# Kernel optimization log

Measured on AMD Instinct MI355X. Metric: run time of the kernel, lower is better.

## Reference

```python
import jax, jax.numpy as jnp
import numpy as np

B, S, D_MODEL = 2, 2048, 1024
HEADS = 16
DK = D_MODEL // HEADS  # 64
Q_RANK, RANK = 6, 2
ROPE_BASE = 10000.0


def _xavier(key, shape):
    # torch nn.init.xavier_uniform_ on weight (out,in); stored here as (in,out)
    fan_in, fan_out = shape
    a = (6.0 / (fan_in + fan_out)) ** 0.5
    return jax.random.uniform(key, shape, jnp.float32, -a, a)


def setup_inputs() -> dict:
    key = jax.random.key(0)
    ks = jax.random.split(key, 10)
    inp = {
        "q": jax.random.normal(ks[0], (B, S, D_MODEL), jnp.float32),
        "k": jax.random.normal(ks[1], (B, S, D_MODEL), jnp.float32),
        "v": jax.random.normal(ks[2], (B, S, D_MODEL), jnp.float32),
        # causal mask; mask==0 -> -inf in scores
        "mask": jnp.tril(jnp.ones((S, S), dtype=bool))[None, None],
        "W_Aq": _xavier(ks[3], (D_MODEL, Q_RANK * HEADS)),
        "W_Ak": _xavier(ks[4], (D_MODEL, RANK * HEADS)),
        "W_Av": _xavier(ks[5], (D_MODEL, RANK * HEADS)),
        "W_Bq": _xavier(ks[6], (D_MODEL, Q_RANK * DK)),
        "W_Bk": _xavier(ks[7], (D_MODEL, RANK * DK)),
        "W_Bv": _xavier(ks[8], (D_MODEL, RANK * DK)),
        "Wo": _xavier(ks[9], (D_MODEL, D_MODEL)),
    }
    return inp


def _rotary_cos_sin(seq_len, dim):
    inv_freq = 1.0 / (ROPE_BASE ** (jnp.arange(0, dim, 2, dtype=jnp.float32) / dim))
    freqs = jnp.outer(jnp.arange(seq_len, dtype=jnp.float32), inv_freq)  # [S, dim/2]
    return jnp.cos(freqs)[None, :, None, :], jnp.sin(freqs)[None, :, None, :]


def _apply_rotary(x, cos, sin):
    # x: [B, S, R, dk]; rotate-half style RoPE
    d = x.shape[-1] // 2
    x1, x2 = x[..., :d], x[..., d:]
    return jnp.concatenate([x1 * cos + x2 * sin, -x1 * sin + x2 * cos], axis=-1)


def reference(q, k, v, mask, W_Aq, W_Ak, W_Av, W_Bq, W_Bk, W_Bv, Wo):
    Bn, Sn, D = q.shape
    # low-rank factor projections
    A_q = (q @ W_Aq).reshape(Bn, Sn, HEADS, Q_RANK)
    A_k = (k @ W_Ak).reshape(Bn, Sn, HEADS, RANK)
    A_v = (v @ W_Av).reshape(Bn, Sn, HEADS, RANK)
    B_q = (q @ W_Bq).reshape(Bn, Sn, Q_RANK, DK)
    B_k = (k @ W_Bk).reshape(Bn, Sn, RANK, DK)
    B_v = (v @ W_Bv).reshape(Bn, Sn, RANK, DK)
    cos, sin = _rotary_cos_sin(Sn, DK)
    B_q = _apply_rotary(B_q, cos, sin)
    B_k = _apply_rotary(B_k, cos, sin)
    # reconstruct per-head q/k/v: [B,H,S,dk]
    qh = jnp.einsum("bshr,bsrd->bhsd", A_q, B_q) / Q_RANK
    kh = jnp.einsum("bshr,bsrd->bhsd", A_k, B_k) / RANK
    vh = jnp.einsum("bshr,bsrd->bhsd", A_v, B_v) / RANK
    # NOTE: original divides by d_k (not sqrt(d_k)) -- faithful to source
    score = jnp.einsum("bhqd,bhkd->bhqk", qh, kh) / DK
    score = jnp.where(mask, score, -jnp.inf)
    # dropout is identity (eval / dropout=0.0)
    att = jax.nn.softmax(score, axis=-1)
    out = jnp.einsum("bhqk,bhkd->bqhd", att, vh).reshape(Bn, Sn, D)
    return out @ Wo
```

## Files before the change

kernel.cpp:

```cpp
#include <hip/hip_runtime.h>
#include <hip/hip_bf16.h>


typedef __attribute__((ext_vector_type(8))) short short8;
typedef __attribute__((ext_vector_type(4))) float floatx4;

#define MFMA16(a, b, c) __builtin_amdgcn_mfma_f32_16x16x32_bf16(a, b, c, 0, 0, 0)

__device__ __forceinline__ float b2f(short s) {
    unsigned int u = ((unsigned int)(unsigned short)s) << 16;
    float f; __builtin_memcpy(&f, &u, 4); return f;
}
__device__ __forceinline__ unsigned short bfbits(float x) {
    __hip_bfloat16 h = __float2bfloat16(x);
    unsigned short u; __builtin_memcpy(&u, &h, 2); return u;
}

__device__ __forceinline__ float wsrc(int n, int k,
                                      const float* __restrict__ Aq, const float* __restrict__ Bq,
                                      const float* __restrict__ Ak, const float* __restrict__ Bk,
                                      const float* __restrict__ Av, const float* __restrict__ Bv,
                                      const float* __restrict__ Wo) {
    if (n < 96) return Aq[(size_t)k * 96 + n];
    if (n < 480) return Bq[(size_t)k * 384 + (n - 96)];
    if (n < 512) return 0.f;
    if (n < 544) return Ak[(size_t)k * 32 + (n - 512)];
    if (n < 672) return Bk[(size_t)k * 128 + (n - 544)];
    if (n < 768) return 0.f;
    if (n < 800) return Av[(size_t)k * 32 + (n - 768)];
    if (n < 928) return Bv[(size_t)k * 128 + (n - 800)];
    if (n < 1024) return 0.f;
    return Wo[(size_t)k * 1024 + (n - 1024)];
}

__global__ __launch_bounds__(256) void pack_wT_kernel(const float* __restrict__ Aq,
                                                      const float* __restrict__ Bq,
                                                      const float* __restrict__ Ak,
                                                      const float* __restrict__ Bk,
                                                      const float* __restrict__ Av,
                                                      const float* __restrict__ Bv,
                                                      const float* __restrict__ Wo,
                                                      __hip_bfloat16* __restrict__ outBase) {
    __shared__ float tile[64][65];
    int k0 = blockIdx.x * 64, n0 = blockIdx.y * 64;
    int tid = threadIdx.x;
#pragma unroll
    for (int p = 0; p < 16; ++p) {
        int idx = p * 256 + tid;
        int kl = idx >> 6, nl = idx & 63;
        tile[kl][nl] = wsrc(n0 + nl, k0 + kl, Aq, Bq, Ak, Bk, Av, Bv, Wo);
    }
    __syncthreads();
#pragma unroll
    for (int p = 0; p < 4; ++p) {
        int idx = p * 256 + tid;
        int nl = idx >> 4, kq = (idx & 15) * 4;
        ushort4 o;
        o.x = bfbits(tile[kq][nl]);
        o.y = bfbits(tile[kq + 1][nl]);
        o.z = bfbits(tile[kq + 2][nl]);
        o.w = bfbits(tile[kq + 3][nl]);
        *(ushort4*)&outBase[(size_t)(n0 + nl) * 1024 + k0 + kq] = o;
    }
}

__global__ __launch_bounds__(256) void gemm3_kernel(const float* __restrict__ q,
                                                    const float* __restrict__ k,
                                                    const float* __restrict__ v,
                                                    const __hip_bfloat16* __restrict__ WT,
                                                    __hip_bfloat16* __restrict__ Pq,
                                                    __hip_bfloat16* __restrict__ Pk,
                                                    __hip_bfloat16* __restrict__ Pv) {
    __shared__ __align__(16) __hip_bfloat16 As[64][72];
    __shared__ __align__(16) __hip_bfloat16 Bs[128][72];
    int lin = blockIdx.x;
    int t = (lin >> 3) & 7;
    int mi = (lin & 7) + ((lin >> 6) << 3);
    int m0 = mi * 64;
    const float* A; __hip_bfloat16* C; int N, n0, wrow;
    if (t < 4)      { A = q; C = Pq; N = 512; n0 = t * 128;        wrow = t * 128; }
    else if (t < 6) { A = k; C = Pk; N = 256; n0 = (t - 4) * 128;  wrow = 512 + (t - 4) * 128; }
    else            { A = v; C = Pv; N = 256; n0 = (t - 6) * 128;  wrow = 768 + (t - 6) * 128; }
    int tid = threadIdx.x;
    int wave = tid >> 6, lane = tid & 63, quad = lane >> 4, l15 = lane & 15;
    floatx4 acc[4][2];
#pragma unroll
    for (int mt = 0; mt < 4; ++mt)
#pragma unroll
        for (int nt = 0; nt < 2; ++nt) acc[mt][nt] = (floatx4){0.f, 0.f, 0.f, 0.f};

    for (int k0 = 0; k0 < 1024; k0 += 64) {
#pragma unroll
        for (int pp = 0; pp < 4; ++pp) {
            int idx = pp * 256 + tid;
            int row = idx >> 4, c4 = (idx & 15) * 4;
            float4 av = *(const float4*)(A + (size_t)(m0 + row) * 1024 + k0 + c4);
            ushort4 bv;
            bv.x = bfbits(av.x); bv.y = bfbits(av.y); bv.z = bfbits(av.z); bv.w = bfbits(av.w);
            *(ushort4*)&As[row][c4] = bv;
        }
#pragma unroll
        for (int pp = 0; pp < 4; ++pp) {
            int idx = pp * 256 + tid;
            int row = idx >> 3, c8 = (idx & 7) * 8;
            *(uint4*)&Bs[row][c8] = *(const uint4*)(WT + (size_t)(wrow + row) * 1024 + k0 + c8);
        }
        __syncthreads();
#pragma unroll
        for (int ks = 0; ks < 64; ks += 32) {
            short8 af[4], bf[2];
#pragma unroll
            for (int mt = 0; mt < 4; ++mt)
                af[mt] = *(const short8*)&As[mt * 16 + l15][ks + quad * 8];
#pragma unroll
            for (int nt = 0; nt < 2; ++nt)
                bf[nt] = *(const short8*)&Bs[wave * 32 + nt * 16 + l15][ks + quad * 8];
#pragma unroll
            for (int mt = 0; mt < 4; ++mt)
#pragma unroll
                for (int nt = 0; nt < 2; ++nt)
                    acc[mt][nt] = MFMA16(af[mt], bf[nt], acc[mt][nt]);
        }
        __syncthreads();
    }
#pragma unroll
    for (int mt = 0; mt < 4; ++mt)
#pragma unroll
        for (int nt = 0; nt < 2; ++nt)
#pragma unroll
            for (int r = 0; r < 4; ++r) {
                int row = m0 + mt * 16 + quad * 4 + r;
                int col = n0 + wave * 32 + nt * 16 + l15;
                C[(size_t)row * N + col] = __float2bfloat16(acc[mt][nt][r]);
            }
}

__global__ __launch_bounds__(256) void gemm_out_kernel(const __hip_bfloat16* __restrict__ A,
                                                       const __hip_bfloat16* __restrict__ BT,
                                                       float* __restrict__ C) {
    __shared__ __align__(16) __hip_bfloat16 As[64][72];
    __shared__ __align__(16) __hip_bfloat16 Bs[128][72];
    int lin = blockIdx.x;
    int n0 = ((lin >> 3) & 7) * 128;
    int mi = (lin & 7) + ((lin >> 6) << 3);
    int m0 = mi * 64;
    int tid = threadIdx.x;
    int wave = tid >> 6, lane = tid & 63, quad = lane >> 4, l15 = lane & 15;
    floatx4 acc[4][2];
#pragma unroll
    for (int mt = 0; mt < 4; ++mt)
#pragma unroll
        for (int nt = 0; nt < 2; ++nt) acc[mt][nt] = (floatx4){0.f, 0.f, 0.f, 0.f};

    for (int k0 = 0; k0 < 1024; k0 += 64) {
#pragma unroll
        for (int pp = 0; pp < 2; ++pp) {
            int idx = pp * 256 + tid;
            int row = idx >> 3, c8 = (idx & 7) * 8;
            *(uint4*)&As[row][c8] = *(const uint4*)(A + (size_t)(m0 + row) * 1024 + k0 + c8);
        }
#pragma unroll
        for (int pp = 0; pp < 4; ++pp) {
            int idx = pp * 256 + tid;
            int row = idx >> 3, c8 = (idx & 7) * 8;
            *(uint4*)&Bs[row][c8] = *(const uint4*)(BT + (size_t)(n0 + row) * 1024 + k0 + c8);
        }
        __syncthreads();
#pragma unroll
        for (int ks = 0; ks < 64; ks += 32) {
            short8 af[4], bf[2];
#pragma unroll
            for (int mt = 0; mt < 4; ++mt)
                af[mt] = *(const short8*)&As[mt * 16 + l15][ks + quad * 8];
#pragma unroll
            for (int nt = 0; nt < 2; ++nt)
                bf[nt] = *(const short8*)&Bs[wave * 32 + nt * 16 + l15][ks + quad * 8];
#pragma unroll
            for (int mt = 0; mt < 4; ++mt)
#pragma unroll
                for (int nt = 0; nt < 2; ++nt)
                    acc[mt][nt] = MFMA16(af[mt], bf[nt], acc[mt][nt]);
        }
        __syncthreads();
    }
#pragma unroll
    for (int mt = 0; mt < 4; ++mt)
#pragma unroll
        for (int nt = 0; nt < 2; ++nt)
#pragma unroll
            for (int r = 0; r < 4; ++r) {
                int row = m0 + mt * 16 + quad * 4 + r;
                int col = n0 + wave * 32 + nt * 16 + l15;
                C[(size_t)row * 1024 + col] = acc[mt][nt][r];
            }
}

__global__ __launch_bounds__(256) void combine_vt_kernel(const __hip_bfloat16* __restrict__ Pq,
                                                         const __hip_bfloat16* __restrict__ Pk,
                                                         const __hip_bfloat16* __restrict__ Pv,
                                                         __hip_bfloat16* __restrict__ qh,
                                                         __hip_bfloat16* __restrict__ kh,
                                                         __hip_bfloat16* __restrict__ vT) {
    __shared__ __align__(16) __hip_bfloat16 LAq[16][96];
    __shared__ __align__(16) __hip_bfloat16 LAk[16][32];
    __shared__ __align__(16) __hip_bfloat16 LAv[16][32];
    __shared__ __align__(16) __hip_bfloat16 LBq[16][6][72];
    __shared__ __align__(16) __hip_bfloat16 LBk[16][2][72];
    __shared__ __align__(16) __hip_bfloat16 LBv[16][2][72];
    int tid = threadIdx.x;
    int token0 = blockIdx.x * 16;
    int b = token0 >> 11, s0 = token0 & 2047, bh0 = b * 16;

    for (int i = tid; i < 16 * 512; i += 256) {
        int s = i >> 9, c = i & 511;
        __hip_bfloat16 val = Pq[(size_t)(token0 + s) * 512 + c];
        if (c < 96) LAq[s][c] = val;
        else if (c < 480) LBq[s][(c - 96) >> 6][(c - 96) & 63] = val;
    }
    for (int i = tid; i < 16 * 256; i += 256) {
        int s = i >> 8, c = i & 255;
        __hip_bfloat16 vk = Pk[(size_t)(token0 + s) * 256 + c];
        __hip_bfloat16 vv = Pv[(size_t)(token0 + s) * 256 + c];
        if (c < 32) { LAk[s][c] = vk; LAv[s][c] = vv; }
        else if (c < 160) {
            LBk[s][(c - 32) >> 6][(c - 32) & 63] = vk;
            LBv[s][(c - 32) >> 6][(c - 32) & 63] = vv;
        }
    }
    __syncthreads();
    for (int i = tid; i < 4096; i += 256) {
        int s = i >> 8, rr = (i >> 5) & 7, d = i & 31;
        float inv = __expf(-(float)d * 0.28782313662425576f);
        float rev = (float)(s0 + s) * inv * 0.15915494309189535f;
        rev -= floorf(rev);
        float sn = __builtin_amdgcn_sinf(rev);
        float cs = __builtin_amdgcn_cosf(rev);
        if (rr < 6) {
            float x1 = b2f(*(short*)&LBq[s][rr][d]), x2 = b2f(*(short*)&LBq[s][rr][d + 32]);
            LBq[s][rr][d] = __float2bfloat16(x1 * cs + x2 * sn);
            LBq[s][rr][d + 32] = __float2bfloat16(-x1 * sn + x2 * cs);
        } else {
            int r2 = rr - 6;
            float x1 = b2f(*(short*)&LBk[s][r2][d]), x2 = b2f(*(short*)&LBk[s][r2][d + 32]);
            LBk[s][r2][d] = __float2bfloat16(x1 * cs + x2 * sn);
            LBk[s][r2][d + 32] = __float2bfloat16(-x1 * sn + x2 * cs);
        }
    }
    __syncthreads();
    const float QSCALE = 1.4426950408889634f / 768.0f;
    {
        int s = tid >> 4, h = tid & 15;
        float aq[6], ak0, ak1;
#pragma unroll
        for (int r = 0; r < 6; ++r) aq[r] = b2f(*(short*)&LAq[s][h * 6 + r]);
        ak0 = b2f(*(short*)&LAk[s][h * 2]);
        ak1 = b2f(*(short*)&LAk[s][h * 2 + 1]);
        size_t obase = ((size_t)(bh0 + h) * 2048 + s0 + s) * 64;
#pragma unroll
        for (int dc = 0; dc < 64; dc += 8) {
            float accq[8] = {0, 0, 0, 0, 0, 0, 0, 0};
#pragma unroll
            for (int r = 0; r < 6; ++r) {
                short8 bq = *(const short8*)&LBq[s][r][dc];
#pragma unroll
                for (int e = 0; e < 8; ++e) accq[e] += aq[r] * b2f(bq[e]);
            }
            short8 bk0 = *(const short8*)&LBk[s][0][dc];
            short8 bk1 = *(const short8*)&LBk[s][1][dc];
            ushort outq[8], outk[8];
#pragma unroll
            for (int e = 0; e < 8; ++e) {
                outq[e] = bfbits(accq[e] * QSCALE);
                outk[e] = bfbits(ak0 * b2f(bk0[e]) + ak1 * b2f(bk1[e]));
            }
            *(uint4*)((__hip_bfloat16*)qh + obase + dc) = *(uint4*)outq;
            *(uint4*)((__hip_bfloat16*)kh + obase + dc) = *(uint4*)outk;
        }
    }
    {
        int s = tid & 15, dg = tid >> 4;
#pragma unroll
        for (int h = 0; h < 16; ++h) {
            float a0 = b2f(*(short*)&LAv[s][h * 2]) * 0.5f;
            float a1 = b2f(*(short*)&LAv[s][h * 2 + 1]) * 0.5f;
#pragma unroll
            for (int dd = 0; dd < 4; ++dd) {
                int d = dg * 4 + dd;
                float val = a0 * b2f(*(short*)&LBv[s][0][d]) + a1 * b2f(*(short*)&LBv[s][1][d]);
                vT[((size_t)(bh0 + h) * 64 + d) * 2048 + s0 + s] = __float2bfloat16(val);
            }
        }
    }
}

__global__ __launch_bounds__(512) void flash_kernel(const __hip_bfloat16* __restrict__ qh,
                                                    const __hip_bfloat16* __restrict__ kh,
                                                    const __hip_bfloat16* __restrict__ vT,
                                                    __hip_bfloat16* __restrict__ att) {
    int lin = blockIdx.x + (blockIdx.y << 5);
    int bh = ((lin & 7) << 2) | ((lin >> 3) & 3);
    int tpair = lin >> 5;
    int tid = threadIdx.x;
    int wave = tid >> 6, lane = tid & 63, quad = lane >> 4, l15 = lane & 15;
    int grp = wave >> 2, wv = wave & 3;
    __shared__ __align__(16) __hip_bfloat16 Ks[2][64][72];
    __shared__ __align__(16) __hip_bfloat16 Vts[2][64][72];
    float* cb = (float*)&Ks[0][0][0];

    int row = tid >> 3, col = (tid & 7) * 8;
    const size_t khb = (size_t)bh * 2048 * 64;
    const size_t vtb = (size_t)bh * 64 * 2048;
    uint4 sk0, sk1, sv0, sv1;
#define FL_ISSUE(P)                                                                  \
    {                                                                                \
        int k0_ = (P) * 128;                                                         \
        sk0 = *(const uint4*)(kh + khb + (size_t)(k0_ + row) * 64 + col);            \
        sk1 = *(const uint4*)(kh + khb + (size_t)(k0_ + 64 + row) * 64 + col);       \
        sv0 = *(const uint4*)(vT + vtb + (size_t)row * 2048 + k0_ + col);            \
        sv1 = *(const uint4*)(vT + vtb + (size_t)row * 2048 + k0_ + 64 + col);       \
    }

    for (int pass = 0; pass < 2; ++pass) {
        int qi = pass ? tpair : (31 - tpair);
        int q0 = qi * 64;
        int npairs = (qi + 2) >> 1;
        const __hip_bfloat16* qrow =
            qh + ((size_t)bh * 2048 + q0 + wv * 16 + l15) * 64 + quad * 8;
        short8 aq0 = *(const short8*)(qrow);
        short8 aq1 = *(const short8*)(qrow + 32);

        floatx4 o[4];
#pragma unroll
        for (int nt = 0; nt < 4; ++nt) o[nt] = (floatx4){0.f, 0.f, 0.f, 0.f};
        float rs = 0.f;
        int qloc = wv * 16 + l15;

        FL_ISSUE(0);
        for (int p = 0; p < npairs; ++p) {
            __syncthreads();
            *(uint4*)&Ks[0][row][col] = sk0;
            *(uint4*)&Ks[1][row][col] = sk1;
            *(uint4*)&Vts[0][row][col] = sv0;
            *(uint4*)&Vts[1][row][col] = sv1;
            __syncthreads();
            if (p + 1 < npairs) FL_ISSUE(p + 1);

            int mytile = 2 * p + grp;
            if (mytile <= qi) {
                floatx4 s[4];
#pragma unroll
                for (int nt = 0; nt < 4; ++nt) s[nt] = (floatx4){0.f, 0.f, 0.f, 0.f};
                __builtin_amdgcn_s_setprio(1);
#pragma unroll
                for (int nt = 0; nt < 4; ++nt) {
                    short8 bk0 = *(const short8*)&Ks[grp][nt * 16 + l15][quad * 8];
                    short8 bk1 = *(const short8*)&Ks[grp][nt * 16 + l15][32 + quad * 8];
                    s[nt] = MFMA16(bk0, aq0, s[nt]);
                    s[nt] = MFMA16(bk1, aq1, s[nt]);
                }
                __builtin_amdgcn_s_setprio(0);
                if (mytile == qi) {
#pragma unroll
                    for (int nt = 0; nt < 4; ++nt) {
                        int kbase = nt * 16 + quad * 4;
#pragma unroll
                        for (int r = 0; r < 4; ++r)
                            if (kbase + r > qloc) s[nt][r] = -__builtin_inff();
                    }
                }
                float pv[4][4];
#pragma unroll
                for (int nt = 0; nt < 4; ++nt)
#pragma unroll
                    for (int r = 0; r < 4; ++r) {
                        pv[nt][r] = exp2f(s[nt][r]);
                        rs += pv[nt][r];
                    }
                union { ushort u[8]; short8 v; } p0, p1;
#pragma unroll
                for (int r = 0; r < 4; ++r) {
                    p0.u[r]     = bfbits(pv[0][r]);
                    p0.u[4 + r] = bfbits(pv[1][r]);
                    p1.u[r]     = bfbits(pv[2][r]);
                    p1.u[4 + r] = bfbits(pv[3][r]);
                }
                __builtin_amdgcn_s_setprio(1);
#pragma unroll
                for (int nt = 0; nt < 4; ++nt) {
                    int vr = nt * 16 + l15;
                    union { ushort4 h[2]; short8 v; } x0, x1;
                    x0.h[0] = *(const ushort4*)&Vts[grp][vr][quad * 4];
                    x0.h[1] = *(const ushort4*)&Vts[grp][vr][16 + quad * 4];
                    x1.h[0] = *(const ushort4*)&Vts[grp][vr][32 + quad * 4];
                    x1.h[1] = *(const ushort4*)&Vts[grp][vr][48 + quad * 4];
                    o[nt] = MFMA16(x0.v, p0.v, o[nt]);
                    o[nt] = MFMA16(x1.v, p1.v, o[nt]);
                }
                __builtin_amdgcn_s_setprio(0);
            }
        }
        __syncthreads();
        int cbase = (wv * 64 + lane) * 17;
        if (grp == 1) {
#pragma unroll
            for (int nt = 0; nt < 4; ++nt)
#pragma unroll
                for (int r = 0; r < 4; ++r) cb[cbase + nt * 4 + r] = o[nt][r];
            cb[cbase + 16] = rs;
        }
        __syncthreads();
        if (grp == 0) {
#pragma unroll
            for (int nt = 0; nt < 4; ++nt)
#pragma unroll
                for (int r = 0; r < 4; ++r) o[nt][r] += cb[cbase + nt * 4 + r];
            rs += cb[cbase + 16];
            rs += __shfl_xor(rs, 16, 64);
            rs += __shfl_xor(rs, 32, 64);
            float inv = 1.0f / rs;
            int b = bh >> 4, h = bh & 15;
            size_t obase = ((size_t)b * 2048 + q0 + wv * 16 + l15) * 1024 + h * 64 + quad * 4;
#pragma unroll
            for (int nt = 0; nt < 4; ++nt) {
                ushort ow[4];
#pragma unroll
                for (int r = 0; r < 4; ++r) ow[r] = bfbits(o[nt][r] * inv);
                *(ushort4*)((__hip_bfloat16*)att + obase + nt * 16) = *(ushort4*)ow;
            }
        }
    }
#undef FL_ISSUE
}

extern "C" void kernel_launch(void* const* d_in, const int* in_sizes, int n_in,
                              void* d_out, int out_size, void* d_ws, size_t ws_size,
                              hipStream_t stream) {
    const float* q = (const float*)d_in[0];
    const float* k = (const float*)d_in[1];
    const float* v = (const float*)d_in[2];
    const float* W_Aq = (const float*)d_in[4];
    const float* W_Ak = (const float*)d_in[5];
    const float* W_Av = (const float*)d_in[6];
    const float* W_Bq = (const float*)d_in[7];
    const float* W_Bk = (const float*)d_in[8];
    const float* W_Bv = (const float*)d_in[9];
    const float* Wo = (const float*)d_in[10];
    float* out = (float*)d_out;

    char* w = (char*)d_ws;
    __hip_bfloat16* qh  = (__hip_bfloat16*)(w + 0);
    __hip_bfloat16* kh  = (__hip_bfloat16*)(w + 8388608);
    __hip_bfloat16* vT  = (__hip_bfloat16*)(w + 16777216);
    __hip_bfloat16* WT  = (__hip_bfloat16*)(w + 25165824);
    __hip_bfloat16* WoT = WT + (size_t)1024 * 1024;
    __hip_bfloat16* Pq  = (__hip_bfloat16*)(w + 29360128);
    __hip_bfloat16* Pk  = (__hip_bfloat16*)(w + 33554432);
    __hip_bfloat16* Pv  = (__hip_bfloat16*)(w + 35651584);
    __hip_bfloat16* att = (__hip_bfloat16*)(w + 37748736);

    pack_wT_kernel<<<dim3(16, 32), 256, 0, stream>>>(W_Aq, W_Bq, W_Ak, W_Bk, W_Av, W_Bv, Wo, WT);
    gemm3_kernel<<<512, 256, 0, stream>>>(q, k, v, WT, Pq, Pk, Pv);
    combine_vt_kernel<<<256, 256, 0, stream>>>(Pq, Pk, Pv, qh, kh, vT);
    flash_kernel<<<dim3(32, 16), 512, 0, stream>>>(qh, kh, vT, att);
    gemm_out_kernel<<<512, 256, 0, stream>>>(att, WoT, out);
}
```

Baseline: 227.1 us.

## Halve GEMM M-tiles and combine token blocks to double grid sizes, vectorize combine loads

The projection and output GEMMs now use 32-row M tiles instead of 64, doubling the block count to 1024 so the 256 CUs are better filled; block-index swizzling is changed to match. The combine kernel handles 8 tokens per block instead of 16, doubling its grid, and its scalar shared-memory staging loads become 16-byte vector loads. The cost is less reuse of each B tile per block, which raises total weight traffic through L2 and LDS, and lower MFMA work per synchronization.

```diff
diff --git a/kernel.cpp b/kernel.cpp
--- a/kernel.cpp
+++ b/kernel.cpp
@@ -71,27 +71,27 @@
                                                     __hip_bfloat16* __restrict__ Pq,
                                                     __hip_bfloat16* __restrict__ Pk,
                                                     __hip_bfloat16* __restrict__ Pv) {
-    __shared__ __align__(16) __hip_bfloat16 As[64][72];
+    __shared__ __align__(16) __hip_bfloat16 As[32][72];
     __shared__ __align__(16) __hip_bfloat16 Bs[128][72];
     int lin = blockIdx.x;
-    int t = (lin >> 3) & 7;
-    int mi = (lin & 7) + ((lin >> 6) << 3);
-    int m0 = mi * 64;
+    int t = lin >> 7;
+    int mi = (lin & 7) + (((lin >> 3) & 15) << 3);
+    int m0 = mi * 32;
     const float* A; __hip_bfloat16* C; int N, n0, wrow;
     if (t < 4)      { A = q; C = Pq; N = 512; n0 = t * 128;        wrow = t * 128; }
     else if (t < 6) { A = k; C = Pk; N = 256; n0 = (t - 4) * 128;  wrow = 512 + (t - 4) * 128; }
     else            { A = v; C = Pv; N = 256; n0 = (t - 6) * 128;  wrow = 768 + (t - 6) * 128; }
     int tid = threadIdx.x;
     int wave = tid >> 6, lane = tid & 63, quad = lane >> 4, l15 = lane & 15;
-    floatx4 acc[4][2];
-#pragma unroll
-    for (int mt = 0; mt < 4; ++mt)
+    floatx4 acc[2][2];
+#pragma unroll
+    for (int mt = 0; mt < 2; ++mt)
 #pragma unroll
         for (int nt = 0; nt < 2; ++nt) acc[mt][nt] = (floatx4){0.f, 0.f, 0.f, 0.f};
 
     for (int k0 = 0; k0 < 1024; k0 += 64) {
 #pragma unroll
-        for (int pp = 0; pp < 4; ++pp) {
+        for (int pp = 0; pp < 2; ++pp) {
             int idx = pp * 256 + tid;
             int row = idx >> 4, c4 = (idx & 15) * 4;
             float4 av = *(const float4*)(A + (size_t)(m0 + row) * 1024 + k0 + c4);
@@ -108,15 +108,15 @@
         __syncthreads();
 #pragma unroll
         for (int ks = 0; ks < 64; ks += 32) {
-            short8 af[4], bf[2];
-#pragma unroll
-            for (int mt = 0; mt < 4; ++mt)
+            short8 af[2], bf[2];
+#pragma unroll
+            for (int mt = 0; mt < 2; ++mt)
                 af[mt] = *(const short8*)&As[mt * 16 + l15][ks + quad * 8];
 #pragma unroll
             for (int nt = 0; nt < 2; ++nt)
                 bf[nt] = *(const short8*)&Bs[wave * 32 + nt * 16 + l15][ks + quad * 8];
 #pragma unroll
-            for (int mt = 0; mt < 4; ++mt)
+            for (int mt = 0; mt < 2; ++mt)
 #pragma unroll
                 for (int nt = 0; nt < 2; ++nt)
                     acc[mt][nt] = MFMA16(af[mt], bf[nt], acc[mt][nt]);
@@ -124,7 +124,7 @@
         __syncthreads();
     }
 #pragma unroll
-    for (int mt = 0; mt < 4; ++mt)
+    for (int mt = 0; mt < 2; ++mt)
 #pragma unroll
         for (int nt = 0; nt < 2; ++nt)
 #pragma unroll
@@ -138,25 +138,23 @@
 __global__ __launch_bounds__(256) void gemm_out_kernel(const __hip_bfloat16* __restrict__ A,
                                                        const __hip_bfloat16* __restrict__ BT,
                                                        float* __restrict__ C) {
-    __shared__ __align__(16) __hip_bfloat16 As[64][72];
+    __shared__ __align__(16) __hip_bfloat16 As[32][72];
     __shared__ __align__(16) __hip_bfloat16 Bs[128][72];
     int lin = blockIdx.x;
-    int n0 = ((lin >> 3) & 7) * 128;
-    int mi = (lin & 7) + ((lin >> 6) << 3);
-    int m0 = mi * 64;
+    int n0 = (lin >> 7) * 128;
+    int mi = (lin & 7) + (((lin >> 3) & 15) << 3);
+    int m0 = mi * 32;
     int tid = threadIdx.x;
     int wave = tid >> 6, lane = tid & 63, quad = lane >> 4, l15 = lane & 15;
-    floatx4 acc[4][2];
-#pragma unroll
-    for (int mt = 0; mt < 4; ++mt)
+    floatx4 acc[2][2];
+#pragma unroll
+    for (int mt = 0; mt < 2; ++mt)
 #pragma unroll
         for (int nt = 0; nt < 2; ++nt) acc[mt][nt] = (floatx4){0.f, 0.f, 0.f, 0.f};
 
     for (int k0 = 0; k0 < 1024; k0 += 64) {
-#pragma unroll
-        for (int pp = 0; pp < 2; ++pp) {
-            int idx = pp * 256 + tid;
-            int row = idx >> 3, c8 = (idx & 7) * 8;
+        {
+            int row = tid >> 3, c8 = (tid & 7) * 8;
             *(uint4*)&As[row][c8] = *(const uint4*)(A + (size_t)(m0 + row) * 1024 + k0 + c8);
         }
 #pragma unroll
@@ -168,15 +166,15 @@
         __syncthreads();
 #pragma unroll
         for (int ks = 0; ks < 64; ks += 32) {
-            short8 af[4], bf[2];
-#pragma unroll
-            for (int mt = 0; mt < 4; ++mt)
+            short8 af[2], bf[2];
+#pragma unroll
+            for (int mt = 0; mt < 2; ++mt)
                 af[mt] = *(const short8*)&As[mt * 16 + l15][ks + quad * 8];
 #pragma unroll
             for (int nt = 0; nt < 2; ++nt)
                 bf[nt] = *(const short8*)&Bs[wave * 32 + nt * 16 + l15][ks + quad * 8];
 #pragma unroll
-            for (int mt = 0; mt < 4; ++mt)
+            for (int mt = 0; mt < 2; ++mt)
 #pragma unroll
                 for (int nt = 0; nt < 2; ++nt)
                     acc[mt][nt] = MFMA16(af[mt], bf[nt], acc[mt][nt]);
@@ -184,7 +182,7 @@
         __syncthreads();
     }
 #pragma unroll
-    for (int mt = 0; mt < 4; ++mt)
+    for (int mt = 0; mt < 2; ++mt)
 #pragma unroll
         for (int nt = 0; nt < 2; ++nt)
 #pragma unroll
@@ -201,34 +199,38 @@
                                                          __hip_bfloat16* __restrict__ qh,
                                                          __hip_bfloat16* __restrict__ kh,
                                                          __hip_bfloat16* __restrict__ vT) {
-    __shared__ __align__(16) __hip_bfloat16 LAq[16][96];
-    __shared__ __align__(16) __hip_bfloat16 LAk[16][32];
-    __shared__ __align__(16) __hip_bfloat16 LAv[16][32];
-    __shared__ __align__(16) __hip_bfloat16 LBq[16][6][72];
-    __shared__ __align__(16) __hip_bfloat16 LBk[16][2][72];
-    __shared__ __align__(16) __hip_bfloat16 LBv[16][2][72];
+    __shared__ __align__(16) __hip_bfloat16 LAq[8][96];
+    __shared__ __align__(16) __hip_bfloat16 LAk[8][32];
+    __shared__ __align__(16) __hip_bfloat16 LAv[8][32];
+    __shared__ __align__(16) __hip_bfloat16 LBq[8][6][72];
+    __shared__ __align__(16) __hip_bfloat16 LBk[8][2][72];
+    __shared__ __align__(16) __hip_bfloat16 LBv[8][2][72];
     int tid = threadIdx.x;
-    int token0 = blockIdx.x * 16;
+    int token0 = blockIdx.x * 8;
     int b = token0 >> 11, s0 = token0 & 2047, bh0 = b * 16;
 
-    for (int i = tid; i < 16 * 512; i += 256) {
-        int s = i >> 9, c = i & 511;
-        __hip_bfloat16 val = Pq[(size_t)(token0 + s) * 512 + c];
-        if (c < 96) LAq[s][c] = val;
-        else if (c < 480) LBq[s][(c - 96) >> 6][(c - 96) & 63] = val;
-    }
-    for (int i = tid; i < 16 * 256; i += 256) {
-        int s = i >> 8, c = i & 255;
-        __hip_bfloat16 vk = Pk[(size_t)(token0 + s) * 256 + c];
-        __hip_bfloat16 vv = Pv[(size_t)(token0 + s) * 256 + c];
-        if (c < 32) { LAk[s][c] = vk; LAv[s][c] = vv; }
-        else if (c < 160) {
-            LBk[s][(c - 32) >> 6][(c - 32) & 63] = vk;
-            LBv[s][(c - 32) >> 6][(c - 32) & 63] = vv;
+#pragma unroll
+    for (int p = 0; p < 2; ++p) {
+        int i = p * 256 + tid;
+        int s = i >> 6, c8 = (i & 63) * 8;
+        uint4 val = *(const uint4*)(Pq + (size_t)(token0 + s) * 512 + c8);
+        if (c8 < 96) *(uint4*)&LAq[s][c8] = val;
+        else if (c8 < 480) *(uint4*)&LBq[s][(c8 - 96) >> 6][(c8 - 96) & 63] = val;
+    }
+    {
+        int s = tid >> 5, c8 = (tid & 31) * 8;
+        uint4 vk = *(const uint4*)(Pk + (size_t)(token0 + s) * 256 + c8);
+        uint4 vv = *(const uint4*)(Pv + (size_t)(token0 + s) * 256 + c8);
+        if (c8 < 32) { *(uint4*)&LAk[s][c8] = vk; *(uint4*)&LAv[s][c8] = vv; }
+        else if (c8 < 160) {
+            *(uint4*)&LBk[s][(c8 - 32) >> 6][(c8 - 32) & 63] = vk;
+            *(uint4*)&LBv[s][(c8 - 32) >> 6][(c8 - 32) & 63] = vv;
         }
     }
     __syncthreads();
-    for (int i = tid; i < 4096; i += 256) {
+#pragma unroll
+    for (int p = 0; p < 8; ++p) {
+        int i = p * 256 + tid;
         int s = i >> 8, rr = (i >> 5) & 7, d = i & 31;
         float inv = __expf(-(float)d * 0.28782313662425576f);
         float rev = (float)(s0 + s) * inv * 0.15915494309189535f;
@@ -249,7 +251,7 @@
     __syncthreads();
     const float QSCALE = 1.4426950408889634f / 768.0f;
     {
-        int s = tid >> 4, h = tid & 15;
+        int s = tid >> 5, h = (tid >> 1) & 15, dh = tid & 1;
         float aq[6], ak0, ak1;
 #pragma unroll
         for (int r = 0; r < 6; ++r) aq[r] = b2f(*(short*)&LAq[s][h * 6 + r]);
@@ -257,7 +259,8 @@
         ak1 = b2f(*(short*)&LAk[s][h * 2 + 1]);
         size_t obase = ((size_t)(bh0 + h) * 2048 + s0 + s) * 64;
 #pragma unroll
-        for (int dc = 0; dc < 64; dc += 8) {
+        for (int dq = 0; dq < 4; ++dq) {
+            int dc = dh * 32 + dq * 8;
             float accq[8] = {0, 0, 0, 0, 0, 0, 0, 0};
 #pragma unroll
             for (int r = 0; r < 6; ++r) {
@@ -278,14 +281,14 @@
         }
     }
     {
-        int s = tid & 15, dg = tid >> 4;
+        int s = tid & 7, dg = tid >> 3;
 #pragma unroll
         for (int h = 0; h < 16; ++h) {
             float a0 = b2f(*(short*)&LAv[s][h * 2]) * 0.5f;
             float a1 = b2f(*(short*)&LAv[s][h * 2 + 1]) * 0.5f;
 #pragma unroll
-            for (int dd = 0; dd < 4; ++dd) {
-                int d = dg * 4 + dd;
+            for (int dd = 0; dd < 2; ++dd) {
+                int d = dg * 2 + dd;
                 float val = a0 * b2f(*(short*)&LBv[s][0][d]) + a1 * b2f(*(short*)&LBv[s][1][d]);
                 vT[((size_t)(bh0 + h) * 64 + d) * 2048 + s0 + s] = __float2bfloat16(val);
             }
@@ -459,8 +462,8 @@
     __hip_bfloat16* att = (__hip_bfloat16*)(w + 37748736);
 
     pack_wT_kernel<<<dim3(16, 32), 256, 0, stream>>>(W_Aq, W_Bq, W_Ak, W_Bk, W_Av, W_Bv, Wo, WT);
-    gemm3_kernel<<<512, 256, 0, stream>>>(q, k, v, WT, Pq, Pk, Pv);
-    combine_vt_kernel<<<256, 256, 0, stream>>>(Pq, Pk, Pv, qh, kh, vT);
+    gemm3_kernel<<<1024, 256, 0, stream>>>(q, k, v, WT, Pq, Pk, Pv);
+    combine_vt_kernel<<<512, 256, 0, stream>>>(Pq, Pk, Pv, qh, kh, vT);
     flash_kernel<<<dim3(32, 16), 512, 0, stream>>>(qh, kh, vT, att);
-    gemm_out_kernel<<<512, 256, 0, stream>>>(att, WoT, out);
-}
+    gemm_out_kernel<<<1024, 256, 0, stream>>>(att, WoT, out);
+}
```

After: 235.8 us. +3.8%, slower.
